# Performance work log

Measured on AMD Instinct MI355X. Metric: run time of the kernel, lower is better.

The kernel has to match this reference:

```python
import jax, jax.numpy as jnp
import numpy as np

N_NODES = 20000
N_EDGES = 8192
UNITS = 128
NUM_GAUSSIANS = 50
CUTOFF = 8.0
GAMMA = 10.0
MIN_DIST, MAX_DIST = 0.0, 30.0


def setup_inputs() -> dict:
    key = jax.random.key(0)
    ks = jax.random.split(key, 6)
    node_features = jax.random.normal(ks[0], (N_NODES, UNITS), dtype=jnp.float32)
    edge_indices = jax.random.randint(ks[1], (2, N_EDGES), 0, N_NODES, dtype=jnp.int32)
    distances = jax.random.uniform(ks[2], (N_EDGES,), dtype=jnp.float32)
    # filter network params (Dense(units) -> swish -> Dense(units*units))
    W1 = jax.random.normal(ks[3], (NUM_GAUSSIANS, UNITS), dtype=jnp.float32) / np.sqrt(NUM_GAUSSIANS)
    b1 = jnp.zeros((UNITS,), dtype=jnp.float32)
    W2 = jax.random.normal(ks[4], (UNITS, UNITS * UNITS), dtype=jnp.float32) / np.sqrt(UNITS)
    b2 = jnp.zeros((UNITS * UNITS,), dtype=jnp.float32)
    # transform Dense(units, use_bias=False)
    Wt = jax.random.normal(ks[5], (UNITS, UNITS), dtype=jnp.float32) / np.sqrt(UNITS)
    return {"node_features": node_features, "edge_indices": edge_indices,
            "distances": distances, "W1": W1, "b1": b1, "W2": W2, "b2": b2, "Wt": Wt}


def reference(node_features, edge_indices, distances, W1, b1, W2, b2, Wt):
    n_nodes, units = node_features.shape
    # cutoff mask (multiplicative; dropped edges contribute zero to the scatter-sum,
    # equivalent to tf.boolean_mask + unsorted_segment_sum)
    mask = (distances <= CUTOFF).astype(node_features.dtype)  # [E]
    # Gaussian basis expansion
    centers = jnp.linspace(MIN_DIST, MAX_DIST, NUM_GAUSSIANS, dtype=jnp.float32)
    df = jnp.exp(-GAMMA * jnp.square(distances[:, None] - centers[None, :]))  # [E, G]
    # filter network: Dense -> swish -> Dense(units*units)
    h = jax.nn.silu(df @ W1 + b1)                    # [E, U]
    filters = (h @ W2 + b2).reshape(-1, units, units)  # [E, U, U]
    # gather source node features, transform, per-edge matvec
    src = node_features[edge_indices[0]]             # [E, U]
    transformed = src @ Wt                           # [E, U]
    filtered = jnp.einsum('eij,ej->ei', filters, transformed) * mask[:, None]  # [E, U]
    # scatter-sum to destination nodes
    messages = jax.ops.segment_sum(filtered, edge_indices[1], num_segments=n_nodes)
    return jax.nn.silu(messages)
```

## Files before the change

kernel.cpp:

```cpp
#include <hip/hip_runtime.h>
#include <hip/hip_fp16.h>


typedef _Float16 f16;
typedef __attribute__((ext_vector_type(8))) f16 f16x8;
typedef __attribute__((ext_vector_type(4))) float f32x4;
typedef __attribute__((ext_vector_type(4))) unsigned int u32x4;

#define NEDGE 8192
#define NNODE 20000
#define NG    50
#define KSTEPS 516
#define W2C_BYTES (KSTEPS * 8192)
#define HT_BYTES (64 * 132 * 128 * 2)
#define TM_BYTES (NEDGE * 128 * 2)

#define LDS_H   0
#define LDS_TM  5120
#define LDS_B   37888
#define LDS_TOT 70656

static __device__ __forceinline__ float fsilu(float x) { return x / (1.0f + __expf(-x)); }

static __device__ __forceinline__ void gll16(const void* g, void* l) {
  __builtin_amdgcn_global_load_lds(
      (const __attribute__((address_space(1))) unsigned int*)g,
      (__attribute__((address_space(3))) unsigned int*)l, 16, 0, 0);
}

__global__ __launch_bounds__(256) void k0_w2c(const float* __restrict__ W2,
                                              const float* __restrict__ b2,
                                              f16* __restrict__ w2c) {
  int gidx = blockIdx.x * 256 + threadIdx.x;
  int lane = gidx & 63;
  int nt   = (gidx >> 6) & 7;
  int step = gidx >> 9;
  int k0i = step * 32 + (lane >> 4) * 8;
  int i   = nt * 16 + (lane & 15);
  int u   = k0i >> 7, j0 = k0i & 127;
  const float* src = (u < 128) ? (W2 + (size_t)u * 16384 + i * 128 + j0)
                               : (b2 + i * 128 + j0);
  union { f16 s[8]; u32x4 v; } pk;
#pragma unroll
  for (int r = 0; r < 8; ++r) pk.s[r] = (f16)src[r];
  *((u32x4*)w2c + gidx) = pk.v;
}

__global__ __launch_bounds__(256) void k1_edge(const float* __restrict__ NF,
                                               const int*   __restrict__ EI,
                                               const float* __restrict__ DI,
                                               const float* __restrict__ W1,
                                               const float* __restrict__ B1,
                                               const float* __restrict__ WT,
                                               f16* __restrict__ ht2,
                                               f16* __restrict__ tmo) {
  __shared__ float df[16][NG];
  __shared__ float s_mask[16];
  __shared__ float s_src[16][128];
  __shared__ float t_tile[16][132];
  __shared__ float h_tile[16][132];
  int et = blockIdx.x, e0 = et * 16, tid = threadIdx.x;

  for (int idx = tid; idx < 16 * NG; idx += 256) {
    int e = idx / NG, g = idx - e * NG;
    float d = DI[e0 + e];
    float x = d - (float)g * (30.0f / 49.0f);
    df[e][g] = __expf(-10.0f * x * x);
  }
  if (tid < 16) s_mask[tid] = (DI[e0 + tid] <= 8.0f) ? 1.0f : 0.0f;
  for (int idx = tid; idx < 16 * 128; idx += 256) {
    int e = idx >> 7, u = idx & 127;
    s_src[e][u] = NF[(size_t)EI[e0 + e] * 128 + u];
  }
  __syncthreads();

  int j = tid & 127, es = tid >> 7;
  for (int e = es * 8; e < es * 8 + 8; ++e) {
    float acc = B1[j];
    for (int g = 0; g < NG; ++g) acc += df[e][g] * W1[g * 128 + j];
    h_tile[e][j] = fsilu(acc);
  }
  {
    float acc[8] = {0.f,0.f,0.f,0.f,0.f,0.f,0.f,0.f};
    for (int u = 0; u < 128; ++u) {
      float wv = WT[u * 128 + j];
#pragma unroll
      for (int e8 = 0; e8 < 8; ++e8) acc[e8] += s_src[es * 8 + e8][u] * wv;
    }
#pragma unroll
    for (int e8 = 0; e8 < 8; ++e8) t_tile[es * 8 + e8][j] = acc[e8];
  }
  __syncthreads();

  int eb = et >> 3, el0 = (et & 7) * 16;
  {
    int u = tid >> 1, hf = tid & 1;
    union { f16 s[8]; u32x4 v; } pk;
#pragma unroll
    for (int k = 0; k < 8; ++k) pk.s[k] = (f16)h_tile[hf * 8 + k][u];
    *(u32x4*)(ht2 + ((size_t)eb * 132 + u) * 128 + el0 + hf * 8) = pk.v;
  }
  if (tid < 16) ht2[((size_t)eb * 132 + 128) * 128 + el0 + tid] = (f16)1.0f;
  {
    int e = tid >> 4, cc = tid & 15;
    float m = s_mask[e];
    union { f16 s[8]; u32x4 v; } pk;
#pragma unroll
    for (int k = 0; k < 8; ++k) pk.s[k] = (f16)(m * t_tile[e][cc * 8 + k]);
    int col = (cc * 16) ^ ((e & 7) << 4);
    *(u32x4*)((char*)tmo + (size_t)(e0 + e) * 256 + col) = pk.v;
  }
}

__global__ __launch_bounds__(256, 2) void k2_gemm(const f16* __restrict__ w2c,
                                                  const f16* __restrict__ ht2,
                                                  const f16* __restrict__ tm,
                                                  const int* __restrict__ EI,
                                                  float* __restrict__ msg) {
  __shared__ u32x4 smem_v[LDS_TOT / 16];
  char* smem = (char*)smem_v;

  const int bid = blockIdx.x;
  const int c   = bid & 7;
  const int eb  = bid >> 3;
  const int e0  = eb * 128;
  const int nu  = (c == 7) ? 17 : 16;
  const int nph = nu * 4;
  const int tid = threadIdx.x, w = tid >> 6, lane = tid & 63;
  const int l15 = lane & 15, g4 = lane >> 4;
  const int wm = w >> 1, wn = w & 1;

  const char* bsrc = (const char*)w2c + (size_t)(c * 64) * 8192;

  {
    const char* tsrc = (const char*)tm + (size_t)e0 * 256 + w * 8192;
#pragma unroll
    for (int q = 0; q < 8; ++q)
      gll16(tsrc + q * 1024 + lane * 16,
            smem + LDS_TM + w * 8192 + q * 1024 + lane * 16);
  }
  if (w == 0) {
    const char* hsrc = (const char*)ht2 + ((size_t)eb * 132 + c * 16) * 256;
#pragma unroll
    for (int q = 0; q < 5; ++q)
      gll16(hsrc + q * 1024 + lane * 16, smem + LDS_H + q * 1024 + lane * 16);
  }
#pragma unroll
  for (int q = 0; q < 2; ++q)
    gll16(bsrc + w * 2048 + q * 1024 + lane * 16,
          smem + LDS_B + w * 2048 + q * 1024 + lane * 16);
#pragma unroll
  for (int q = 0; q < 2; ++q)
    gll16(bsrc + 8192 + w * 2048 + q * 1024 + lane * 16,
          smem + LDS_B + 8192 + w * 2048 + q * 1024 + lane * 16);
  asm volatile("s_waitcnt vmcnt(2)" ::: "memory");
  __builtin_amdgcn_s_barrier();

  f32x4 acc[4][4];
#pragma unroll
  for (int rt = 0; rt < 4; ++rt)
#pragma unroll
    for (int nt = 0; nt < 4; ++nt) acc[rt][nt] = (f32x4){0.f, 0.f, 0.f, 0.f};

  const int tmbase = LDS_TM + (wm * 64 + l15) * 256;
  const int colsw  = (l15 & 7) << 4;
  const int bcol   = wn * 4096 + lane * 16;
  const __half* hbase = (const __half*)(smem + LDS_H) + wm * 64 + l15;

  for (int u = 0; u < nu; ++u) {
    __half2 h2[4];
#pragma unroll
    for (int rt = 0; rt < 4; ++rt) h2[rt] = __half2half2(hbase[u * 128 + rt * 16]);
#pragma unroll
    for (int jc = 0; jc < 4; ++jc) {
      const int p = u * 4 + jc;
      int ps = p + 2; ps = (ps < nph) ? ps : (nph - 1);
      const char* ns = bsrc + (size_t)ps * 8192 + w * 2048;
      char* nd = smem + LDS_B + ((jc + 2) & 3) * 8192 + w * 2048;
      gll16(ns + lane * 16, nd + lane * 16);
      gll16(ns + 1024 + lane * 16, nd + 1024 + lane * 16);
      union uf { f16x8 v; __half2 h[4]; };
      uf a[4];
#pragma unroll
      for (int rt = 0; rt < 4; ++rt) {
        uf t;
        t.v = *(const f16x8*)(smem + tmbase + rt * 4096 + ((jc * 64 + g4 * 16) ^ colsw));
#pragma unroll
        for (int q = 0; q < 4; ++q) a[rt].h[q] = __hmul2(t.h[q], h2[rt]);
      }
      f16x8 b[4];
#pragma unroll
      for (int nt = 0; nt < 4; ++nt)
        b[nt] = *(const f16x8*)(smem + LDS_B + jc * 8192 + bcol + nt * 1024);
      __builtin_amdgcn_s_setprio(1);
#pragma unroll
      for (int nt = 0; nt < 4; ++nt)
#pragma unroll
        for (int rt = 0; rt < 4; ++rt)
          acc[rt][nt] = __builtin_amdgcn_mfma_f32_16x16x32_f16(a[rt].v, b[nt], acc[rt][nt], 0, 0, 0);
      __builtin_amdgcn_s_setprio(0);
      asm volatile("s_waitcnt vmcnt(2)" ::: "memory");
      __builtin_amdgcn_s_barrier();
    }
  }

  const int* dst = EI + NEDGE;
#pragma unroll
  for (int rt = 0; rt < 4; ++rt) {
#pragma unroll
    for (int r = 0; r < 4; ++r) {
      int e = e0 + wm * 64 + rt * 16 + g4 * 4 + r;
      float* row = msg + (size_t)dst[e] * 128 + wn * 64 + l15;
#pragma unroll
      for (int nt = 0; nt < 4; ++nt)
        atomicAdd(row + nt * 16, acc[rt][nt][r]);
    }
  }
}

__global__ __launch_bounds__(256) void k3_silu(float* __restrict__ out, int n4) {
  int idx = blockIdx.x * 256 + threadIdx.x;
  int stride = gridDim.x * 256;
  f32x4* p = (f32x4*)out;
  for (; idx < n4; idx += stride) {
    f32x4 v = p[idx];
#pragma unroll
    for (int cc = 0; cc < 4; ++cc) v[cc] = fsilu(v[cc]);
    p[idx] = v;
  }
}

extern "C" void kernel_launch(void* const* d_in, const int* in_sizes, int n_in,
                              void* d_out, int out_size, void* d_ws, size_t ws_size,
                              hipStream_t stream) {
  const float* NF = (const float*)d_in[0];
  const int*   EI = (const int*)  d_in[1];
  const float* DI = (const float*)d_in[2];
  const float* W1 = (const float*)d_in[3];
  const float* B1 = (const float*)d_in[4];
  const float* W2 = (const float*)d_in[5];
  const float* B2 = (const float*)d_in[6];
  const float* WT = (const float*)d_in[7];
  float* out = (float*)d_out;

  f16* w2c = (f16*)d_ws;
  f16* ht2 = (f16*)((char*)d_ws + W2C_BYTES);
  f16* tmo = (f16*)((char*)d_ws + W2C_BYTES + HT_BYTES);
  size_t needed = (size_t)W2C_BYTES + HT_BYTES + TM_BYTES;
  if (ws_size < needed) return;

  hipMemsetAsync(d_out, 0, (size_t)out_size * sizeof(float), stream);
  k0_w2c <<<dim3(1032), dim3(256), 0, stream>>>(W2, B2, w2c);
  k1_edge<<<dim3(512),  dim3(256), 0, stream>>>(NF, EI, DI, W1, B1, WT, ht2, tmo);
  k2_gemm<<<dim3(512),  dim3(256), 0, stream>>>(w2c, ht2, tmo, EI, out);
  k3_silu<<<dim3(1024), dim3(256), 0, stream>>>(out, out_size / 4);
}
```

Baseline: 96.60 us.

## Stream W2 filter tiles directly into registers and keep node tile resident

The GEMM kernel no longer stages W2 tiles in LDS through async global-to-LDS copies with a per-step barrier. Each wave now loads its B fragments straight from global memory into registers, double-buffered one step ahead. The transformed-node A tile is read from LDS into registers once and reused across all K steps, and the per-step barriers are removed. The cost is that the two waves sharing a column half both load the same B data, only one step of global latency is hidden, register pressure rises, and the final prefetch reads one step past the end of the W2 buffer.

```diff
diff --git a/kernel.cpp b/kernel.cpp
--- a/kernel.cpp
+++ b/kernel.cpp
@@ -17,8 +17,7 @@
 
 #define LDS_H   0
 #define LDS_TM  5120
-#define LDS_B   37888
-#define LDS_TOT 70656
+#define LDS_TOT 37888
 
 static __device__ __forceinline__ float fsilu(float x) { return x / (1.0f + __expf(-x)); }
 
@@ -125,13 +124,10 @@
   const int eb  = bid >> 3;
   const int e0  = eb * 128;
   const int nu  = (c == 7) ? 17 : 16;
-  const int nph = nu * 4;
   const int tid = threadIdx.x, w = tid >> 6, lane = tid & 63;
   const int l15 = lane & 15, g4 = lane >> 4;
   const int wm = w >> 1, wn = w & 1;
 
-  const char* bsrc = (const char*)w2c + (size_t)(c * 64) * 8192;
-
   {
     const char* tsrc = (const char*)tm + (size_t)e0 * 256 + w * 8192;
 #pragma unroll
@@ -145,16 +141,30 @@
     for (int q = 0; q < 5; ++q)
       gll16(hsrc + q * 1024 + lane * 16, smem + LDS_H + q * 1024 + lane * 16);
   }
-#pragma unroll
-  for (int q = 0; q < 2; ++q)
-    gll16(bsrc + w * 2048 + q * 1024 + lane * 16,
-          smem + LDS_B + w * 2048 + q * 1024 + lane * 16);
-#pragma unroll
-  for (int q = 0; q < 2; ++q)
-    gll16(bsrc + 8192 + w * 2048 + q * 1024 + lane * 16,
-          smem + LDS_B + 8192 + w * 2048 + q * 1024 + lane * 16);
-  asm volatile("s_waitcnt vmcnt(2)" ::: "memory");
-  __builtin_amdgcn_s_barrier();
+  __syncthreads();
+
+  f16x8 Tall[4][4];
+  {
+    const int tmrow = LDS_TM + (wm * 64 + l15) * 256;
+    const int colsw = (l15 & 7) << 4;
+#pragma unroll
+    for (int rt = 0; rt < 4; ++rt)
+#pragma unroll
+      for (int jc = 0; jc < 4; ++jc)
+        Tall[rt][jc] = *(const f16x8*)(smem + tmrow + rt * 4096 +
+                                       ((jc * 64 + g4 * 16) ^ colsw));
+  }
+  const __half* hbase = (const __half*)(smem + LDS_H) + wm * 64 + l15;
+
+  __half2 hc[4], hn[4];
+#pragma unroll
+  for (int rt = 0; rt < 4; ++rt) hc[rt] = __half2half2(hbase[rt * 16]);
+
+  const char* bp = (const char*)w2c + (size_t)(c * 64) * 8192 + wn * 4096 + lane * 16;
+  f16x8 Bc[4], Bn[4];
+#pragma unroll
+  for (int nt = 0; nt < 4; ++nt) Bn[nt] = *(const f16x8*)(bp + nt * 1024);
+  bp += 8192;
 
   f32x4 acc[4][4];
 #pragma unroll
@@ -162,46 +172,37 @@
 #pragma unroll
     for (int nt = 0; nt < 4; ++nt) acc[rt][nt] = (f32x4){0.f, 0.f, 0.f, 0.f};
 
-  const int tmbase = LDS_TM + (wm * 64 + l15) * 256;
-  const int colsw  = (l15 & 7) << 4;
-  const int bcol   = wn * 4096 + lane * 16;
-  const __half* hbase = (const __half*)(smem + LDS_H) + wm * 64 + l15;
-
   for (int u = 0; u < nu; ++u) {
-    __half2 h2[4];
-#pragma unroll
-    for (int rt = 0; rt < 4; ++rt) h2[rt] = __half2half2(hbase[u * 128 + rt * 16]);
 #pragma unroll
     for (int jc = 0; jc < 4; ++jc) {
-      const int p = u * 4 + jc;
-      int ps = p + 2; ps = (ps < nph) ? ps : (nph - 1);
-      const char* ns = bsrc + (size_t)ps * 8192 + w * 2048;
-      char* nd = smem + LDS_B + ((jc + 2) & 3) * 8192 + w * 2048;
-      gll16(ns + lane * 16, nd + lane * 16);
-      gll16(ns + 1024 + lane * 16, nd + 1024 + lane * 16);
+#pragma unroll
+      for (int nt = 0; nt < 4; ++nt) Bc[nt] = Bn[nt];
+#pragma unroll
+      for (int nt = 0; nt < 4; ++nt) Bn[nt] = *(const f16x8*)(bp + nt * 1024);
+      bp += 8192;
+      if (jc == 1) {
+#pragma unroll
+        for (int rt = 0; rt < 4; ++rt)
+          hn[rt] = __half2half2(hbase[(u + 1) * 128 + rt * 16]);
+      }
       union uf { f16x8 v; __half2 h[4]; };
       uf a[4];
 #pragma unroll
       for (int rt = 0; rt < 4; ++rt) {
-        uf t;
-        t.v = *(const f16x8*)(smem + tmbase + rt * 4096 + ((jc * 64 + g4 * 16) ^ colsw));
-#pragma unroll
-        for (int q = 0; q < 4; ++q) a[rt].h[q] = __hmul2(t.h[q], h2[rt]);
+        uf t; t.v = Tall[rt][jc];
+#pragma unroll
+        for (int q = 0; q < 4; ++q) a[rt].h[q] = __hmul2(t.h[q], hc[rt]);
       }
-      f16x8 b[4];
+      __builtin_amdgcn_s_setprio(1);
 #pragma unroll
       for (int nt = 0; nt < 4; ++nt)
-        b[nt] = *(const f16x8*)(smem + LDS_B + jc * 8192 + bcol + nt * 1024);
-      __builtin_amdgcn_s_setprio(1);
-#pragma unroll
-      for (int nt = 0; nt < 4; ++nt)
 #pragma unroll
         for (int rt = 0; rt < 4; ++rt)
-          acc[rt][nt] = __builtin_amdgcn_mfma_f32_16x16x32_f16(a[rt].v, b[nt], acc[rt][nt], 0, 0, 0);
+          acc[rt][nt] = __builtin_amdgcn_mfma_f32_16x16x32_f16(a[rt].v, Bc[nt], acc[rt][nt], 0, 0, 0);
       __builtin_amdgcn_s_setprio(0);
-      asm volatile("s_waitcnt vmcnt(2)" ::: "memory");
-      __builtin_amdgcn_s_barrier();
     }
+#pragma unroll
+    for (int rt = 0; rt < 4; ++rt) hc[rt] = hn[rt];
   }
 
   const int* dst = EI + NEDGE;
```

Result: faster. 89.63 us (-7.2%).
